# Kernel tuning notes

Measured on AMD Instinct MI355X. Metric: run time of the kernel, lower is better.

## Reference

```python
import jax, jax.numpy as jnp
import numpy as np

L, E, H, V = 12, 1024, 4096, 50277
LN_EPS = 9.999999747378752e-06  # tf float32 1e-5


def _layernorm(x, w, b):
    m = jnp.mean(x)
    xc = x - m
    return xc / jnp.sqrt(jnp.mean(xc * xc) + LN_EPS) * w + b


def setup_inputs() -> dict:
    key = jax.random.key(0)
    ks = jax.random.split(key, 32)
    f32 = jnp.float32

    def n(i, shape, s=0.02):
        return (jax.random.normal(ks[i], shape, f32) * s).astype(f32)

    inp = {
        "statea": n(0, (L, E), 0.3),
        "stateb": jax.random.uniform(ks[1], (L, E), f32),
        "statec": jax.random.uniform(ks[2], (L, E), f32),
        "stated": n(3, (L, E), 0.3),
        "preprocess": n(4, (V, E), 0.5),
        "ln1w": 1.0 + n(5, (L, E), 0.05),
        "ln1b": n(6, (L, E), 0.05),
        "ln2w": 1.0 + n(7, (L, E), 0.05),
        "ln2b": n(8, (L, E), 0.05),
        "att_key": n(9, (L, E, E)),
        "att_receptance": n(10, (L, E, E)),
        "att_value": n(11, (L, E, E)),
        "kktk": jax.random.uniform(ks[12], (L, E), f32),
        "vvtv": jax.random.uniform(ks[13], (L, E), f32),
        "rrtr": jax.random.uniform(ks[14], (L, E), f32),
        "time_first": n(15, (L, E), 0.2),
        "time_decay": n(16, (L, E), 0.2) - 1.0,
        "outputvv": n(17, (L, E, E)),
        "time_mix_k_ffn": jax.random.uniform(ks[18], (L, E), f32),
        "time_mix_r_ffn": jax.random.uniform(ks[19], (L, E), f32),
        "key_ffn": n(20, (L, H, E)),
        "receptance_ffn": n(21, (L, E, E)),
        "value_ffn": n(22, (L, E, H)),
        "post0": 1.0 + n(23, (E,), 0.05),
        "post1": n(24, (E,), 0.05),
        "post2": n(25, (V, E)),
        "token": 123,
    }
    return inp


def _forward(statea, stateb, statec, stated, preprocess, ln1w, ln1b, ln2w, ln2b,
             att_key, att_receptance, att_value, kktk, vvtv, rrtr, time_first,
             time_decay, outputvv, time_mix_k_ffn, time_mix_r_ffn, key_ffn,
             receptance_ffn, value_ffn, post0, post1, post2, token):
    x0 = preprocess[token]  # [E]

    def step(x, p):
        (sa, sb, sc, sd, l1w, l1b, l2w, l2b, ak, ar, av, kk, vv, rr,
         tfirst, tdecay, ovv, tmk_m, tmr_m, kf, rf, vf) = p
        xy = _layernorm(x, l1w, l1b)
        # WKV time-mixing (single step): mat-vecs + exp-decay state recursion
        k = jnp.exp(ak @ (xy + kk * sa))        # [E]
        v = av @ (xy + vv * sa)                 # [E]
        r = jnp.exp(ar @ (xy + rr * sa)) + 1.0  # [E]
        etf = jnp.exp(tfirst)
        w = sb + etf * k * v
        d = sc * r + etf * k * r
        mvv = ovv @ (w / (d + 0.001))           # [E]
        sxx = x + mvv
        aaa = xy
        etd = jnp.exp(tdecay)
        bbb = sb * etd + k * v
        ccc = sc * etd + k
        # channel-mixing FFN
        xx = _layernorm(sxx, l2w, l2b)
        kma = kf @ (xx + tmk_m * sd)            # [H]
        km = jnp.square(jnp.maximum(kma, 0.0))
        rt = jnp.exp(rf @ (xx + tmr_m * sd)) + 1.0  # [E]
        x_new = sxx + (vf @ km) / rt
        ddd = xx
        return x_new, (aaa, bbb, ccc, ddd)

    xs = (statea, stateb, statec, stated, ln1w, ln1b, ln2w, ln2b, att_key,
          att_receptance, att_value, kktk, vvtv, rrtr, time_first, time_decay,
          outputvv, time_mix_k_ffn, time_mix_r_ffn, key_ffn, receptance_ffn,
          value_ffn)
    xL, (aaa, bbb, ccc, ddd) = jax.lax.scan(step, x0, xs)
    logits = post2 @ _layernorm(xL, post0, post1)  # [V]
    return logits, aaa, bbb, ccc, ddd


def reference(statea, stateb, statec, stated, preprocess, ln1w, ln1b, ln2w, ln2b,
              att_key, att_receptance, att_value, kktk, vvtv, rrtr, time_first,
              time_decay, outputvv, time_mix_k_ffn, time_mix_r_ffn, key_ffn,
              receptance_ffn, value_ffn, post0, post1, post2, token):
    return _forward(statea, stateb, statec, stated, preprocess, ln1w, ln1b,
                    ln2w, ln2b, att_key, att_receptance, att_value, kktk, vvtv,
                    rrtr, time_first, time_decay, outputvv, time_mix_k_ffn,
                    time_mix_r_ffn, key_ffn, receptance_ffn, value_ffn, post0,
                    post1, post2, token)
```

## Files before the change

kernel.cpp:

```cpp
#include <hip/hip_runtime.h>
#include <math.h>


constexpr int E = 1024;
constexpr int H = 4096;
constexpr int V = 50277;
constexpr int L = 12;
constexpr int NBLK = 256;
constexpr int NTHR = 512;
constexpr float LN_EPS = 9.999999747378752e-06f;

#define SCOPE_AGENT __HIP_MEMORY_SCOPE_AGENT

__device__ __forceinline__ void cstoref(float *p, float v) {
  __hip_atomic_store(p, v, __ATOMIC_RELAXED, SCOPE_AGENT);
}
__device__ __forceinline__ void cstoreu(unsigned *p, unsigned v) {
  __hip_atomic_store(p, v, __ATOMIC_RELAXED, SCOPE_AGENT);
}
__device__ __forceinline__ unsigned cloadu(const unsigned *p) {
  return __hip_atomic_load(p, __ATOMIC_RELAXED, SCOPE_AGENT);
}
__device__ __forceinline__ float2 cload2(const float *p) {
  union { unsigned long long u; float2 f; } c;
  c.u = __hip_atomic_load((const unsigned long long *)p, __ATOMIC_RELAXED, SCOPE_AGENT);
  return c.f;
}

__device__ __forceinline__ void lds_sync() {
  __builtin_amdgcn_sched_barrier(0);
  asm volatile("s_waitcnt lgkmcnt(0)" ::: "memory");
  __builtin_amdgcn_s_barrier();
  __builtin_amdgcn_sched_barrier(0);
}

struct Args {
  const float *statea, *stateb, *statec, *stated, *pre;
  const float *ln1w, *ln1b, *ln2w, *ln2b;
  const float *ak, *ar, *av, *kk, *vv, *rr, *tf, *td, *ovv;
  const float *tmk, *tmr, *kf, *rf, *vf;
  const float *post0, *post1, *post2;
  const int *token;
  float *out;
  float *ws;
  unsigned *flags;
};

__device__ __forceinline__ void bar_arrive(const Args &a, unsigned ep, int blk) {
  __syncthreads();
  if (threadIdx.x == 0) cstoreu(&a.flags[blk * 32], ep);
  __builtin_amdgcn_sched_barrier(0);
}

__device__ __forceinline__ void bar_spin(const Args &a, unsigned ep) {
  __builtin_amdgcn_sched_barrier(0);
  if (threadIdx.x < NBLK) {
    while (cloadu(&a.flags[threadIdx.x * 32]) < ep)
      __builtin_amdgcn_s_sleep(2);
  }
  __builtin_amdgcn_s_barrier();
  __builtin_amdgcn_sched_barrier(0);
}

__device__ __forceinline__ float wred(float v) {
#pragma unroll
  for (int off = 32; off; off >>= 1) v += __shfl_down(v, off, 64);
  return v;
}

__device__ __forceinline__ float dot4(float4 w, float4 x) {
  return w.x * x.x + w.y * x.y + w.z * x.z + w.w * x.w;
}

__device__ __forceinline__ float2 block_stats_v(float2 v, float *s_x, float *s_red,
                                                int tid, int lane, int wid) {
  reinterpret_cast<float2 *>(s_x)[tid] = v;
  float s = v.x + v.y, s2 = v.x * v.x + v.y * v.y;
#pragma unroll
  for (int off = 32; off; off >>= 1) {
    s += __shfl_down(s, off, 64);
    s2 += __shfl_down(s2, off, 64);
  }
  if (lane == 0) { s_red[wid] = s; s_red[8 + wid] = s2; }
  lds_sync();
  float ts = 0.f, ts2 = 0.f;
#pragma unroll
  for (int i = 0; i < 8; ++i) { ts += s_red[i]; ts2 += s_red[8 + i]; }
  float m = ts * (1.0f / E);
  float var = ts2 * (1.0f / E) - m * m;
  return make_float2(m, rsqrtf(var + LN_EPS));
}

__device__ __forceinline__ void loadrow(float4 *d, const float4 *P, int r, int lane) {
  const float4 *p = P + (size_t)r * 256;
  d[0] = p[lane]; d[1] = p[lane + 64]; d[2] = p[lane + 128]; d[3] = p[lane + 192];
}

__global__ __launch_bounds__(NTHR) void rwkv_fused(Args a) {
  __shared__ __align__(16) float s_a[4096];
  __shared__ __align__(16) float s_x[1024];
  __shared__ __align__(16) float s_y[1024];
  __shared__ float s_pp[24];
  __shared__ float s_red[16];
  __shared__ float s_rt[4];

  const int tid = threadIdx.x;
  const int lane = tid & 63;
  const int wid = tid >> 6;
  const int blk = blockIdx.x;
  const int rloc = wid >> 1;
  const int h = wid & 1;
  const int grow = blk * 4 + rloc;
  const int b0h = h * 128 + lane;
  const int bv = h * 512 + lane;

  float *ws_u = a.ws, *ws_sxx = a.ws + 1024, *ws_x = a.ws + 2048, *ws_km = a.ws + 3072;
  float *out_logits = a.out;
  float *out_aaa = a.out + V;
  float *out_bbb = out_aaa + L * E;
  float *out_ccc = out_bbb + L * E;
  float *out_ddd = out_ccc + L * E;

  const int tok = a.token[0];
  const float *pre_row = a.pre + (size_t)tok * E;
  const float4 *s4a = reinterpret_cast<const float4 *>(s_a);

  unsigned ep = 1;

  float4 pw1[6];
  float2 e1w, e1b, e1sa, e1kk, e1vv, e1rr;
  float e_tf = 0.f, e_td = 0.f, e_sb = 0.f, e_sc = 0.f;

  {
    const float4 *kr = reinterpret_cast<const float4 *>(a.ak + (size_t)grow * E);
    const float4 *vr = reinterpret_cast<const float4 *>(a.av + (size_t)grow * E);
    const float4 *rr4 = reinterpret_cast<const float4 *>(a.ar + (size_t)grow * E);
    pw1[0] = kr[b0h]; pw1[1] = kr[b0h + 64];
    pw1[2] = vr[b0h]; pw1[3] = vr[b0h + 64];
    pw1[4] = rr4[b0h]; pw1[5] = rr4[b0h + 64];
    e1w = reinterpret_cast<const float2 *>(a.ln1w)[tid];
    e1b = reinterpret_cast<const float2 *>(a.ln1b)[tid];
    e1sa = reinterpret_cast<const float2 *>(a.statea)[tid];
    e1kk = reinterpret_cast<const float2 *>(a.kk)[tid];
    e1vv = reinterpret_cast<const float2 *>(a.vv)[tid];
    e1rr = reinterpret_cast<const float2 *>(a.rr)[tid];
    if (tid < 4) {
      size_t o = (size_t)blk * 4 + tid;
      e_tf = a.tf[o]; e_td = a.td[o]; e_sb = a.stateb[o]; e_sc = a.statec[o];
    }
  }

#pragma unroll 1
  for (int l = 0; l < L; ++l) {
    const size_t lE = (size_t)l * E;
    float4 pw2[2], pw3[10], pw4[8];
    float2 e3w, e3b, e3sd, e3tk, e3tr;

    {
      float2 v;
      if (l == 0) v = reinterpret_cast<const float2 *>(pre_row)[tid];
      else        v = cload2(ws_x + 2 * tid);
      {
        const float4 *orow = reinterpret_cast<const float4 *>(a.ovv + (lE + grow) * E);
        pw2[0] = orow[b0h]; pw2[1] = orow[b0h + 64];
        const float *kfb = a.kf + (size_t)l * H * E;
        const float4 *k0 = reinterpret_cast<const float4 *>(kfb + (size_t)(blk * 16 + wid) * E);
        pw3[0] = k0[lane];       pw3[1] = k0[lane + 64];
        pw3[2] = k0[lane + 128]; pw3[3] = k0[lane + 192];
      }
      float2 st = block_stats_v(v, s_x, s_red, tid, lane, wid);
      float2 xy = make_float2((v.x - st.x) * st.y * e1w.x + e1b.x,
                              (v.y - st.x) * st.y * e1w.y + e1b.y);
      reinterpret_cast<float2 *>(s_y)[tid] = xy;
      reinterpret_cast<float2 *>(s_a)[tid] =
          make_float2(xy.x + e1kk.x * e1sa.x, xy.y + e1kk.y * e1sa.y);
      reinterpret_cast<float2 *>(s_a + 1024)[tid] =
          make_float2(xy.x + e1vv.x * e1sa.x, xy.y + e1vv.y * e1sa.y);
      reinterpret_cast<float2 *>(s_a + 2048)[tid] =
          make_float2(xy.x + e1rr.x * e1sa.x, xy.y + e1rr.y * e1sa.y);
      lds_sync();
      float accK = dot4(pw1[0], s4a[b0h]) + dot4(pw1[1], s4a[b0h + 64]);
      float accV = dot4(pw1[2], s4a[256 + b0h]) + dot4(pw1[3], s4a[256 + b0h + 64]);
      float accR = dot4(pw1[4], s4a[512 + b0h]) + dot4(pw1[5], s4a[512 + b0h + 64]);
      accK = wred(accK); accV = wred(accV); accR = wred(accR);
      if (lane == 0) {
        s_pp[wid * 3 + 0] = accK;
        s_pp[wid * 3 + 1] = accV;
        s_pp[wid * 3 + 2] = accR;
      }
      lds_sync();
      if (tid < 4) {
        size_t o = lE + blk * 4 + tid;
        float K = s_pp[(2 * tid) * 3] + s_pp[(2 * tid + 1) * 3];
        float Vv = s_pp[(2 * tid) * 3 + 1] + s_pp[(2 * tid + 1) * 3 + 1];
        float R = s_pp[(2 * tid) * 3 + 2] + s_pp[(2 * tid + 1) * 3 + 2];
        float kx = expf(K), rx = expf(R) + 1.0f;
        float etf = expf(e_tf), etd = expf(e_td);
        float w_ = e_sb + etf * kx * Vv;
        float d_ = e_sc * rx + etf * kx * rx;
        cstoref(&ws_u[blk * 4 + tid], w_ / (d_ + 0.001f));
        out_bbb[o] = e_sb * etd + kx * Vv;
        out_ccc[o] = e_sc * etd + kx;
        out_aaa[o] = s_y[blk * 4 + tid];
      }
    }
    bar_arrive(a, ep, blk);
    {
      const float *kfb = a.kf + (size_t)l * H * E;
      const float4 *k1 = reinterpret_cast<const float4 *>(kfb + (size_t)(blk * 16 + 8 + wid) * E);
      pw3[4] = k1[lane];       pw3[5] = k1[lane + 64];
      pw3[6] = k1[lane + 128]; pw3[7] = k1[lane + 192];
    }
    bar_spin(a, ep); ++ep;

    {
      float2 u2 = cload2(ws_u + 2 * tid);
      {
        const float4 *rrow = reinterpret_cast<const float4 *>(a.rf + (lE + grow) * E);
        pw3[8] = rrow[b0h]; pw3[9] = rrow[b0h + 64];
        e3w = reinterpret_cast<const float2 *>(a.ln2w + lE)[tid];
        e3b = reinterpret_cast<const float2 *>(a.ln2b + lE)[tid];
        e3sd = reinterpret_cast<const float2 *>(a.stated + lE)[tid];
        e3tk = reinterpret_cast<const float2 *>(a.tmk + lE)[tid];
        e3tr = reinterpret_cast<const float2 *>(a.tmr + lE)[tid];
        const float4 *vrow = reinterpret_cast<const float4 *>(a.vf + (lE + grow) * H);
        pw4[0] = vrow[bv];       pw4[1] = vrow[bv + 64];
        pw4[2] = vrow[bv + 128]; pw4[3] = vrow[bv + 192];
      }
      reinterpret_cast<float2 *>(s_a)[tid] = u2;
      lds_sync();
      float acc = dot4(pw2[0], s4a[b0h]) + dot4(pw2[1], s4a[b0h + 64]);
      acc = wred(acc);
      if (lane == 0) s_pp[wid] = acc;
      lds_sync();
      if (tid < 4) {
        float sxx = s_x[blk * 4 + tid] + s_pp[2 * tid] + s_pp[2 * tid + 1];
        cstoref(&ws_sxx[blk * 4 + tid], sxx);
      }
    }
    bar_arrive(a, ep, blk);
    {
      const float4 *vrow = reinterpret_cast<const float4 *>(a.vf + (lE + grow) * H);
      pw4[4] = vrow[bv + 256]; pw4[5] = vrow[bv + 320];
      pw4[6] = vrow[bv + 384]; pw4[7] = vrow[bv + 448];
    }
    bar_spin(a, ep); ++ep;

    {
      float2 vsx = cload2(ws_sxx + 2 * tid);
      if (l + 1 < L) {
        const size_t nE = (size_t)(l + 1) * E;
        const float4 *kr = reinterpret_cast<const float4 *>(a.ak + (nE + grow) * E);
        const float4 *vr = reinterpret_cast<const float4 *>(a.av + (nE + grow) * E);
        const float4 *rr4 = reinterpret_cast<const float4 *>(a.ar + (nE + grow) * E);
        pw1[0] = kr[b0h]; pw1[1] = kr[b0h + 64];
        pw1[2] = vr[b0h]; pw1[3] = vr[b0h + 64];
        pw1[4] = rr4[b0h]; pw1[5] = rr4[b0h + 64];
        e1w = reinterpret_cast<const float2 *>(a.ln1w + nE)[tid];
        e1b = reinterpret_cast<const float2 *>(a.ln1b + nE)[tid];
        e1sa = reinterpret_cast<const float2 *>(a.statea + nE)[tid];
        e1kk = reinterpret_cast<const float2 *>(a.kk + nE)[tid];
        e1vv = reinterpret_cast<const float2 *>(a.vv + nE)[tid];
        e1rr = reinterpret_cast<const float2 *>(a.rr + nE)[tid];
        if (tid < 4) {
          size_t o = nE + blk * 4 + tid;
          e_tf = a.tf[o]; e_td = a.td[o]; e_sb = a.stateb[o]; e_sc = a.statec[o];
        }
      } else {
        e1w = reinterpret_cast<const float2 *>(a.post0)[tid];
        e1b = reinterpret_cast<const float2 *>(a.post1)[tid];
      }
      float2 st = block_stats_v(vsx, s_x, s_red, tid, lane, wid);
      float2 xx = make_float2((vsx.x - st.x) * st.y * e3w.x + e3b.x,
                              (vsx.y - st.x) * st.y * e3w.y + e3b.y);
      reinterpret_cast<float2 *>(s_y)[tid] = xx;
      reinterpret_cast<float2 *>(s_a)[tid] =
          make_float2(xx.x + e3tk.x * e3sd.x, xx.y + e3tk.y * e3sd.y);
      reinterpret_cast<float2 *>(s_a + 1024)[tid] =
          make_float2(xx.x + e3tr.x * e3sd.x, xx.y + e3tr.y * e3sd.y);
      lds_sync();
      float k0 = dot4(pw3[0], s4a[lane]) + dot4(pw3[1], s4a[lane + 64]) +
                 dot4(pw3[2], s4a[lane + 128]) + dot4(pw3[3], s4a[lane + 192]);
      float k1 = dot4(pw3[4], s4a[lane]) + dot4(pw3[5], s4a[lane + 64]) +
                 dot4(pw3[6], s4a[lane + 128]) + dot4(pw3[7], s4a[lane + 192]);
      float ar_ = dot4(pw3[8], s4a[256 + b0h]) + dot4(pw3[9], s4a[256 + b0h + 64]);
      k0 = wred(k0); k1 = wred(k1); ar_ = wred(ar_);
      if (lane == 0) {
        float t0 = fmaxf(k0, 0.f), t1v = fmaxf(k1, 0.f);
        cstoref(&ws_km[blk * 16 + wid], t0 * t0);
        cstoref(&ws_km[blk * 16 + 8 + wid], t1v * t1v);
        s_pp[wid] = ar_;
      }
      lds_sync();
      if (tid < 4) {
        s_rt[tid] = expf(s_pp[2 * tid] + s_pp[2 * tid + 1]) + 1.0f;
        out_ddd[lE + blk * 4 + tid] = s_y[blk * 4 + tid];
      }
    }
    bar_arrive(a, ep, blk);
    bar_spin(a, ep); ++ep;

    {
      float2 k0a = cload2(ws_km + 4 * tid);
      float2 k0b = cload2(ws_km + 4 * tid + 2);
      float2 k1a = cload2(ws_km + 2048 + 4 * tid);
      float2 k1b = cload2(ws_km + 2048 + 4 * tid + 2);
      reinterpret_cast<float2 *>(s_a)[2 * tid] = k0a;
      reinterpret_cast<float2 *>(s_a)[2 * tid + 1] = k0b;
      reinterpret_cast<float2 *>(s_a)[1024 + 2 * tid] = k1a;
      reinterpret_cast<float2 *>(s_a)[1024 + 2 * tid + 1] = k1b;
      lds_sync();
      float acc = dot4(pw4[0], s4a[bv]) + dot4(pw4[1], s4a[bv + 64]) +
                  dot4(pw4[2], s4a[bv + 128]) + dot4(pw4[3], s4a[bv + 192]) +
                  dot4(pw4[4], s4a[bv + 256]) + dot4(pw4[5], s4a[bv + 320]) +
                  dot4(pw4[6], s4a[bv + 384]) + dot4(pw4[7], s4a[bv + 448]);
      acc = wred(acc);
      if (lane == 0) s_pp[wid] = acc;
      lds_sync();
      if (tid < 4) {
        float xn = s_x[blk * 4 + tid] + (s_pp[2 * tid] + s_pp[2 * tid + 1]) / s_rt[tid];
        cstoref(&ws_x[blk * 4 + tid], xn);
      }
    }
    bar_arrive(a, ep, blk);
    bar_spin(a, ep); ++ep;
  }

  {
    float2 v = cload2(ws_x + 2 * tid);
    float2 st = block_stats_v(v, s_x, s_red, tid, lane, wid);
    reinterpret_cast<float2 *>(s_a)[tid] =
        make_float2((v.x - st.x) * st.y * e1w.x + e1b.x,
                    (v.y - st.x) * st.y * e1w.y + e1b.y);
    lds_sync();

    const float4 *P2 = reinterpret_cast<const float4 *>(a.post2);
    const int gw = blk * 8 + wid;
    int r0 = gw, r1 = gw + 2048;
    float4 A0[4], A1[4];
    loadrow(A0, P2, r0, lane);
    loadrow(A1, P2, r1 < V ? r1 : r0, lane);
    while (true) {
      int n0 = r0 + 4096, n1 = n0 + 2048;
      bool more = n0 < V;
      float4 B0[4], B1[4];
      if (more) {
        loadrow(B0, P2, n0, lane);
        loadrow(B1, P2, n1 < V ? n1 : n0, lane);
      }
      float a0 = dot4(A0[0], s4a[lane]) + dot4(A0[1], s4a[lane + 64]) +
                 dot4(A0[2], s4a[lane + 128]) + dot4(A0[3], s4a[lane + 192]);
      float a1 = dot4(A1[0], s4a[lane]) + dot4(A1[1], s4a[lane + 64]) +
                 dot4(A1[2], s4a[lane + 128]) + dot4(A1[3], s4a[lane + 192]);
      a0 = wred(a0); a1 = wred(a1);
      if (lane == 0) {
        out_logits[r0] = a0;
        if (r1 < V) out_logits[r1] = a1;
      }
      if (!more) break;
#pragma unroll
      for (int q = 0; q < 4; ++q) { A0[q] = B0[q]; A1[q] = B1[q]; }
      r0 = n0; r1 = n1;
    }
  }
}

extern "C" void kernel_launch(void *const *d_in, const int *in_sizes, int n_in,
                              void *d_out, int out_size, void *d_ws, size_t ws_size,
                              hipStream_t stream) {
  (void)in_sizes; (void)n_in; (void)out_size; (void)ws_size;
  Args a;
  a.statea = (const float *)d_in[0];
  a.stateb = (const float *)d_in[1];
  a.statec = (const float *)d_in[2];
  a.stated = (const float *)d_in[3];
  a.pre    = (const float *)d_in[4];
  a.ln1w   = (const float *)d_in[5];
  a.ln1b   = (const float *)d_in[6];
  a.ln2w   = (const float *)d_in[7];
  a.ln2b   = (const float *)d_in[8];
  a.ak     = (const float *)d_in[9];
  a.ar     = (const float *)d_in[10];
  a.av     = (const float *)d_in[11];
  a.kk     = (const float *)d_in[12];
  a.vv     = (const float *)d_in[13];
  a.rr     = (const float *)d_in[14];
  a.tf     = (const float *)d_in[15];
  a.td     = (const float *)d_in[16];
  a.ovv    = (const float *)d_in[17];
  a.tmk    = (const float *)d_in[18];
  a.tmr    = (const float *)d_in[19];
  a.kf     = (const float *)d_in[20];
  a.rf     = (const float *)d_in[21];
  a.vf     = (const float *)d_in[22];
  a.post0  = (const float *)d_in[23];
  a.post1  = (const float *)d_in[24];
  a.post2  = (const float *)d_in[25];
  a.token  = (const int *)d_in[26];
  a.out    = (float *)d_out;

  a.flags  = (unsigned *)d_ws;
  a.ws     = (float *)((char *)d_ws + 32768);

  hipMemsetAsync(d_ws, 0, 32768, stream);
  rwkv_fused<<<NBLK, NTHR, 0, stream>>>(a);
}
```

Before: 266.8 us.

## Replace grid flag barriers with epoch-tagged data words and partial LN stats

Drops the per-phase grid barrier (flag arrive plus spin over all blocks). Each published value now carries a 64-bit word with its epoch in the high half, so consumers poll only the exact data they need until it is current. Blocks also publish partial sums and sums of squares for the residual vectors, so layernorm statistics come from the gathered partials without a second block reduction. Weight prefetch placement changes, and launch bounds now request two blocks per CU. This removes barrier round trips but doubles the size of every exchanged word and adds polling traffic on many addresses.

```diff
diff --git a/kernel.cpp b/kernel.cpp
--- a/kernel.cpp
+++ b/kernel.cpp
@@ -1,6 +1,8 @@
 #include <hip/hip_runtime.h>
 #include <math.h>
 
+
+typedef unsigned long long u64;
 
 constexpr int E = 1024;
 constexpr int H = 4096;
@@ -12,26 +14,23 @@
 
 #define SCOPE_AGENT __HIP_MEMORY_SCOPE_AGENT
 
-__device__ __forceinline__ void cstoref(float *p, float v) {
+__device__ __forceinline__ u64 aload(const u64 *p) {
+  return __hip_atomic_load(p, __ATOMIC_RELAXED, SCOPE_AGENT);
+}
+__device__ __forceinline__ void astore(u64 *p, u64 v) {
   __hip_atomic_store(p, v, __ATOMIC_RELAXED, SCOPE_AGENT);
 }
-__device__ __forceinline__ void cstoreu(unsigned *p, unsigned v) {
-  __hip_atomic_store(p, v, __ATOMIC_RELAXED, SCOPE_AGENT);
-}
-__device__ __forceinline__ unsigned cloadu(const unsigned *p) {
-  return __hip_atomic_load(p, __ATOMIC_RELAXED, SCOPE_AGENT);
-}
-__device__ __forceinline__ float2 cload2(const float *p) {
-  union { unsigned long long u; float2 f; } c;
-  c.u = __hip_atomic_load((const unsigned long long *)p, __ATOMIC_RELAXED, SCOPE_AGENT);
-  return c.f;
+__device__ __forceinline__ u64 mkw(unsigned ep, float f) {
+  return ((u64)ep << 32) | (u64)__float_as_uint(f);
+}
+__device__ __forceinline__ float wpay(u64 v) { return __uint_as_float((unsigned)v); }
+__device__ __forceinline__ bool freshw(u64 v, unsigned ep) {
+  return (unsigned)(v >> 32) == ep;
 }
 
 __device__ __forceinline__ void lds_sync() {
-  __builtin_amdgcn_sched_barrier(0);
   asm volatile("s_waitcnt lgkmcnt(0)" ::: "memory");
   __builtin_amdgcn_s_barrier();
-  __builtin_amdgcn_sched_barrier(0);
 }
 
 struct Args {
@@ -42,25 +41,8 @@
   const float *post0, *post1, *post2;
   const int *token;
   float *out;
-  float *ws;
-  unsigned *flags;
+  u64 *wu, *wsx, *ssx, *wkm, *wx, *sxs;
 };
-
-__device__ __forceinline__ void bar_arrive(const Args &a, unsigned ep, int blk) {
-  __syncthreads();
-  if (threadIdx.x == 0) cstoreu(&a.flags[blk * 32], ep);
-  __builtin_amdgcn_sched_barrier(0);
-}
-
-__device__ __forceinline__ void bar_spin(const Args &a, unsigned ep) {
-  __builtin_amdgcn_sched_barrier(0);
-  if (threadIdx.x < NBLK) {
-    while (cloadu(&a.flags[threadIdx.x * 32]) < ep)
-      __builtin_amdgcn_s_sleep(2);
-  }
-  __builtin_amdgcn_s_barrier();
-  __builtin_amdgcn_sched_barrier(0);
-}
 
 __device__ __forceinline__ float wred(float v) {
 #pragma unroll
@@ -72,36 +54,115 @@
   return w.x * x.x + w.y * x.y + w.z * x.z + w.w * x.w;
 }
 
-__device__ __forceinline__ float2 block_stats_v(float2 v, float *s_x, float *s_red,
-                                                int tid, int lane, int wid) {
-  reinterpret_cast<float2 *>(s_x)[tid] = v;
-  float s = v.x + v.y, s2 = v.x * v.x + v.y * v.y;
-#pragma unroll
-  for (int off = 32; off; off >>= 1) {
-    s += __shfl_down(s, off, 64);
-    s2 += __shfl_down(s2, off, 64);
-  }
-  if (lane == 0) { s_red[wid] = s; s_red[8 + wid] = s2; }
+__device__ __forceinline__ float2 gather2(const u64 *wd, unsigned ep, int tid) {
+  const u64 *p = wd + 2 * tid;
+  u64 a0 = aload(p), a1 = aload(p + 1);
+  while (!(freshw(a0, ep) & freshw(a1, ep))) {
+    __builtin_amdgcn_s_sleep(1);
+    a0 = aload(p); a1 = aload(p + 1);
+  }
+  return make_float2(wpay(a0), wpay(a1));
+}
+
+__device__ __forceinline__ void gather2s(const u64 *wd, const u64 *st, unsigned ep,
+                                         int tid, float2 &v, float &sp) {
+  const u64 *p = wd + 2 * tid;
+  const u64 *q = st + tid;
+  u64 a0 = aload(p), a1 = aload(p + 1), a2 = aload(q);
+  while (!(freshw(a0, ep) & freshw(a1, ep) & freshw(a2, ep))) {
+    __builtin_amdgcn_s_sleep(1);
+    a0 = aload(p); a1 = aload(p + 1); a2 = aload(q);
+  }
+  v = make_float2(wpay(a0), wpay(a1));
+  sp = wpay(a2);
+}
+
+__device__ __forceinline__ void gather8(const u64 *wd, unsigned ep, int tid,
+                                        float4 &f0, float4 &f1) {
+  const u64 *p = wd + 8 * tid;
+  u64 b0, b1, b2, b3, b4, b5, b6, b7;
+  for (;;) {
+    b0 = aload(p);     b1 = aload(p + 1); b2 = aload(p + 2); b3 = aload(p + 3);
+    b4 = aload(p + 4); b5 = aload(p + 5); b6 = aload(p + 6); b7 = aload(p + 7);
+    bool ok = freshw(b0, ep) & freshw(b1, ep) & freshw(b2, ep) & freshw(b3, ep) &
+              freshw(b4, ep) & freshw(b5, ep) & freshw(b6, ep) & freshw(b7, ep);
+    if (ok) break;
+    __builtin_amdgcn_s_sleep(1);
+  }
+  f0 = make_float4(wpay(b0), wpay(b1), wpay(b2), wpay(b3));
+  f1 = make_float4(wpay(b4), wpay(b5), wpay(b6), wpay(b7));
+}
+
+__device__ __forceinline__ float2 stats_from_partials(float sp, float *s_red,
+                                                      int lane, int wid) {
+#pragma unroll
+  for (int m = 2; m <= 32; m <<= 1) sp += __shfl_xor(sp, m, 64);
+  if (lane < 2) s_red[wid * 2 + lane] = sp;
   lds_sync();
   float ts = 0.f, ts2 = 0.f;
 #pragma unroll
-  for (int i = 0; i < 8; ++i) { ts += s_red[i]; ts2 += s_red[8 + i]; }
+  for (int i = 0; i < 8; ++i) { ts += s_red[2 * i]; ts2 += s_red[2 * i + 1]; }
   float m = ts * (1.0f / E);
   float var = ts2 * (1.0f / E) - m * m;
   return make_float2(m, rsqrtf(var + LN_EPS));
 }
 
+__device__ __forceinline__ float2 stats_full(float2 v, float *s_red, int lane, int wid) {
+  float s = v.x + v.y, s2 = v.x * v.x + v.y * v.y;
+#pragma unroll
+  for (int m = 1; m <= 32; m <<= 1) {
+    s += __shfl_xor(s, m, 64);
+    s2 += __shfl_xor(s2, m, 64);
+  }
+  if (lane == 0) { s_red[wid * 2] = s; s_red[wid * 2 + 1] = s2; }
+  lds_sync();
+  float ts = 0.f, ts2 = 0.f;
+#pragma unroll
+  for (int i = 0; i < 8; ++i) { ts += s_red[2 * i]; ts2 += s_red[2 * i + 1]; }
+  float m = ts * (1.0f / E);
+  float var = ts2 * (1.0f / E) - m * m;
+  return make_float2(m, rsqrtf(var + LN_EPS));
+}
+
+struct P1B {
+  float4 w[6];
+  float2 lw, lb, sa, kk, vv, rr;
+  float tf, td, sb, sc;
+};
+
+__device__ __forceinline__ void load_p1(P1B &p, const Args &a, int l, int grow,
+                                        int b0h, int tid, int blk) {
+  const size_t lE = (size_t)l * E;
+  const float4 *kr = reinterpret_cast<const float4 *>(a.ak + (lE + grow) * E);
+  const float4 *vr = reinterpret_cast<const float4 *>(a.av + (lE + grow) * E);
+  const float4 *rr4 = reinterpret_cast<const float4 *>(a.ar + (lE + grow) * E);
+  p.w[0] = kr[b0h]; p.w[1] = kr[b0h + 64];
+  p.w[2] = vr[b0h]; p.w[3] = vr[b0h + 64];
+  p.w[4] = rr4[b0h]; p.w[5] = rr4[b0h + 64];
+  p.lw = reinterpret_cast<const float2 *>(a.ln1w + lE)[tid];
+  p.lb = reinterpret_cast<const float2 *>(a.ln1b + lE)[tid];
+  p.sa = reinterpret_cast<const float2 *>(a.statea + lE)[tid];
+  p.kk = reinterpret_cast<const float2 *>(a.kk + lE)[tid];
+  p.vv = reinterpret_cast<const float2 *>(a.vv + lE)[tid];
+  p.rr = reinterpret_cast<const float2 *>(a.rr + lE)[tid];
+  if (tid < 4) {
+    size_t o = lE + blk * 4 + tid;
+    p.tf = a.tf[o]; p.td = a.td[o]; p.sb = a.stateb[o]; p.sc = a.statec[o];
+  } else {
+    p.tf = 0.f; p.td = 0.f; p.sb = 0.f; p.sc = 1.f;
+  }
+}
+
 __device__ __forceinline__ void loadrow(float4 *d, const float4 *P, int r, int lane) {
   const float4 *p = P + (size_t)r * 256;
   d[0] = p[lane]; d[1] = p[lane + 64]; d[2] = p[lane + 128]; d[3] = p[lane + 192];
 }
 
-__global__ __launch_bounds__(NTHR) void rwkv_fused(Args a) {
+__global__ __launch_bounds__(NTHR, 2) void rwkv_fused(Args a) {
   __shared__ __align__(16) float s_a[4096];
   __shared__ __align__(16) float s_x[1024];
-  __shared__ __align__(16) float s_y[1024];
+  __shared__ float s_red[16];
   __shared__ float s_pp[24];
-  __shared__ float s_red[16];
   __shared__ float s_rt[4];
 
   const int tid = threadIdx.x;
@@ -114,7 +175,6 @@
   const int b0h = h * 128 + lane;
   const int bv = h * 512 + lane;
 
-  float *ws_u = a.ws, *ws_sxx = a.ws + 1024, *ws_x = a.ws + 2048, *ws_km = a.ws + 3072;
   float *out_logits = a.out;
   float *out_aaa = a.out + V;
   float *out_bbb = out_aaa + L * E;
@@ -125,63 +185,44 @@
   const float *pre_row = a.pre + (size_t)tok * E;
   const float4 *s4a = reinterpret_cast<const float4 *>(s_a);
 
-  unsigned ep = 1;
-
-  float4 pw1[6];
-  float2 e1w, e1b, e1sa, e1kk, e1vv, e1rr;
-  float e_tf = 0.f, e_td = 0.f, e_sb = 0.f, e_sc = 0.f;
-
-  {
-    const float4 *kr = reinterpret_cast<const float4 *>(a.ak + (size_t)grow * E);
-    const float4 *vr = reinterpret_cast<const float4 *>(a.av + (size_t)grow * E);
-    const float4 *rr4 = reinterpret_cast<const float4 *>(a.ar + (size_t)grow * E);
-    pw1[0] = kr[b0h]; pw1[1] = kr[b0h + 64];
-    pw1[2] = vr[b0h]; pw1[3] = vr[b0h + 64];
-    pw1[4] = rr4[b0h]; pw1[5] = rr4[b0h + 64];
-    e1w = reinterpret_cast<const float2 *>(a.ln1w)[tid];
-    e1b = reinterpret_cast<const float2 *>(a.ln1b)[tid];
-    e1sa = reinterpret_cast<const float2 *>(a.statea)[tid];
-    e1kk = reinterpret_cast<const float2 *>(a.kk)[tid];
-    e1vv = reinterpret_cast<const float2 *>(a.vv)[tid];
-    e1rr = reinterpret_cast<const float2 *>(a.rr)[tid];
-    if (tid < 4) {
-      size_t o = (size_t)blk * 4 + tid;
-      e_tf = a.tf[o]; e_td = a.td[o]; e_sb = a.stateb[o]; e_sc = a.statec[o];
-    }
-  }
+  P1B p1;
+  load_p1(p1, a, 0, grow, b0h, tid, blk);
 
 #pragma unroll 1
   for (int l = 0; l < L; ++l) {
     const size_t lE = (size_t)l * E;
-    float4 pw2[2], pw3[10], pw4[8];
+    const unsigned e1 = 4 * l + 1, e2 = 4 * l + 2, e3 = 4 * l + 3, e4 = 4 * l + 4;
+    float4 pwo[2], pw3[10], pw4[8];
     float2 e3w, e3b, e3sd, e3tk, e3tr;
 
     {
-      float2 v;
-      if (l == 0) v = reinterpret_cast<const float2 *>(pre_row)[tid];
-      else        v = cload2(ws_x + 2 * tid);
-      {
-        const float4 *orow = reinterpret_cast<const float4 *>(a.ovv + (lE + grow) * E);
-        pw2[0] = orow[b0h]; pw2[1] = orow[b0h + 64];
-        const float *kfb = a.kf + (size_t)l * H * E;
-        const float4 *k0 = reinterpret_cast<const float4 *>(kfb + (size_t)(blk * 16 + wid) * E);
-        pw3[0] = k0[lane];       pw3[1] = k0[lane + 64];
-        pw3[2] = k0[lane + 128]; pw3[3] = k0[lane + 192];
-      }
-      float2 st = block_stats_v(v, s_x, s_red, tid, lane, wid);
-      float2 xy = make_float2((v.x - st.x) * st.y * e1w.x + e1b.x,
-                              (v.y - st.x) * st.y * e1w.y + e1b.y);
-      reinterpret_cast<float2 *>(s_y)[tid] = xy;
+      float2 xv; float2 st;
+      if (l == 0) {
+        xv = reinterpret_cast<const float2 *>(pre_row)[tid];
+        reinterpret_cast<float2 *>(s_x)[tid] = xv;
+        st = stats_full(xv, s_red, lane, wid);
+      } else {
+        float sp;
+        gather2s(a.wx, a.sxs, 4 * l, tid, xv, sp);
+        reinterpret_cast<float2 *>(s_x)[tid] = xv;
+        st = stats_from_partials(sp, s_red, lane, wid);
+      }
+      float2 xy = make_float2((xv.x - st.x) * st.y * p1.lw.x + p1.lb.x,
+                              (xv.y - st.x) * st.y * p1.lw.y + p1.lb.y);
+      if ((tid >> 1) == blk) {
+        out_aaa[lE + 2 * tid] = xy.x;
+        out_aaa[lE + 2 * tid + 1] = xy.y;
+      }
       reinterpret_cast<float2 *>(s_a)[tid] =
-          make_float2(xy.x + e1kk.x * e1sa.x, xy.y + e1kk.y * e1sa.y);
+          make_float2(xy.x + p1.kk.x * p1.sa.x, xy.y + p1.kk.y * p1.sa.y);
       reinterpret_cast<float2 *>(s_a + 1024)[tid] =
-          make_float2(xy.x + e1vv.x * e1sa.x, xy.y + e1vv.y * e1sa.y);
+          make_float2(xy.x + p1.vv.x * p1.sa.x, xy.y + p1.vv.y * p1.sa.y);
       reinterpret_cast<float2 *>(s_a + 2048)[tid] =
-          make_float2(xy.x + e1rr.x * e1sa.x, xy.y + e1rr.y * e1sa.y);
-      lds_sync();
-      float accK = dot4(pw1[0], s4a[b0h]) + dot4(pw1[1], s4a[b0h + 64]);
-      float accV = dot4(pw1[2], s4a[256 + b0h]) + dot4(pw1[3], s4a[256 + b0h + 64]);
-      float accR = dot4(pw1[4], s4a[512 + b0h]) + dot4(pw1[5], s4a[512 + b0h + 64]);
+          make_float2(xy.x + p1.rr.x * p1.sa.x, xy.y + p1.rr.y * p1.sa.y);
+      lds_sync();
+      float accK = dot4(p1.w[0], s4a[b0h]) + dot4(p1.w[1], s4a[b0h + 64]);
+      float accV = dot4(p1.w[2], s4a[256 + b0h]) + dot4(p1.w[3], s4a[256 + b0h + 64]);
+      float accR = dot4(p1.w[4], s4a[512 + b0h]) + dot4(p1.w[5], s4a[512 + b0h + 64]);
       accK = wred(accK); accV = wred(accV); accR = wred(accR);
       if (lane == 0) {
         s_pp[wid * 3 + 0] = accK;
@@ -189,33 +230,46 @@
         s_pp[wid * 3 + 2] = accR;
       }
       lds_sync();
-      if (tid < 4) {
-        size_t o = lE + blk * 4 + tid;
-        float K = s_pp[(2 * tid) * 3] + s_pp[(2 * tid + 1) * 3];
-        float Vv = s_pp[(2 * tid) * 3 + 1] + s_pp[(2 * tid + 1) * 3 + 1];
-        float R = s_pp[(2 * tid) * 3 + 2] + s_pp[(2 * tid + 1) * 3 + 2];
+      {
+        const float4 *orow = reinterpret_cast<const float4 *>(a.ovv + (lE + grow) * E);
+        pwo[0] = orow[b0h]; pwo[1] = orow[b0h + 64];
+      }
+      if (wid == 0) {
+        int i = lane & 3;
+        float K = s_pp[(2 * i) * 3] + s_pp[(2 * i + 1) * 3];
+        float Vv = s_pp[(2 * i) * 3 + 1] + s_pp[(2 * i + 1) * 3 + 1];
+        float R = s_pp[(2 * i) * 3 + 2] + s_pp[(2 * i + 1) * 3 + 2];
         float kx = expf(K), rx = expf(R) + 1.0f;
-        float etf = expf(e_tf), etd = expf(e_td);
-        float w_ = e_sb + etf * kx * Vv;
-        float d_ = e_sc * rx + etf * kx * rx;
-        cstoref(&ws_u[blk * 4 + tid], w_ / (d_ + 0.001f));
-        out_bbb[o] = e_sb * etd + kx * Vv;
-        out_ccc[o] = e_sc * etd + kx;
-        out_aaa[o] = s_y[blk * 4 + tid];
+        float etf = expf(p1.tf), etd = expf(p1.td);
+        float w_ = p1.sb + etf * kx * Vv;
+        float d_ = p1.sc * rx + etf * kx * rx;
+        float uv = w_ / (d_ + 0.001f);
+        if (lane < 4) {
+          size_t o = lE + blk * 4 + lane;
+          astore(a.wu + blk * 4 + lane, mkw(e1, uv));
+          out_bbb[o] = p1.sb * etd + kx * Vv;
+          out_ccc[o] = p1.sc * etd + kx;
+        }
       }
     }
-    bar_arrive(a, ep, blk);
+
     {
-      const float *kfb = a.kf + (size_t)l * H * E;
-      const float4 *k1 = reinterpret_cast<const float4 *>(kfb + (size_t)(blk * 16 + 8 + wid) * E);
-      pw3[4] = k1[lane];       pw3[5] = k1[lane + 64];
-      pw3[6] = k1[lane + 128]; pw3[7] = k1[lane + 192];
-    }
-    bar_spin(a, ep); ++ep;
-
-    {
-      float2 u2 = cload2(ws_u + 2 * tid);
+      float2 u2 = gather2(a.wu, e1, tid);
+      reinterpret_cast<float2 *>(s_a)[tid] = u2;
+      lds_sync();
+      float acc = dot4(pwo[0], s4a[b0h]) + dot4(pwo[1], s4a[b0h + 64]);
+      float x4 = s_x[blk * 4 + (lane & 3)];
+      acc = wred(acc);
+      if (lane == 0) s_pp[wid] = acc;
+      lds_sync();
       {
+        const float *kfb = a.kf + (size_t)l * H * E;
+        const float4 *k0 = reinterpret_cast<const float4 *>(kfb + (size_t)(blk * 16 + wid) * E);
+        const float4 *k1 = reinterpret_cast<const float4 *>(kfb + (size_t)(blk * 16 + 8 + wid) * E);
+        pw3[0] = k0[lane];       pw3[1] = k0[lane + 64];
+        pw3[2] = k0[lane + 128]; pw3[3] = k0[lane + 192];
+        pw3[4] = k1[lane];       pw3[5] = k1[lane + 64];
+        pw3[6] = k1[lane + 128]; pw3[7] = k1[lane + 192];
         const float4 *rrow = reinterpret_cast<const float4 *>(a.rf + (lE + grow) * E);
         pw3[8] = rrow[b0h]; pw3[9] = rrow[b0h + 64];
         e3w = reinterpret_cast<const float2 *>(a.ln2w + lE)[tid];
@@ -223,115 +277,102 @@
         e3sd = reinterpret_cast<const float2 *>(a.stated + lE)[tid];
         e3tk = reinterpret_cast<const float2 *>(a.tmk + lE)[tid];
         e3tr = reinterpret_cast<const float2 *>(a.tmr + lE)[tid];
-        const float4 *vrow = reinterpret_cast<const float4 *>(a.vf + (lE + grow) * H);
-        pw4[0] = vrow[bv];       pw4[1] = vrow[bv + 64];
-        pw4[2] = vrow[bv + 128]; pw4[3] = vrow[bv + 192];
-      }
-      reinterpret_cast<float2 *>(s_a)[tid] = u2;
-      lds_sync();
-      float acc = dot4(pw2[0], s4a[b0h]) + dot4(pw2[1], s4a[b0h + 64]);
-      acc = wred(acc);
-      if (lane == 0) s_pp[wid] = acc;
-      lds_sync();
-      if (tid < 4) {
-        float sxx = s_x[blk * 4 + tid] + s_pp[2 * tid] + s_pp[2 * tid + 1];
-        cstoref(&ws_sxx[blk * 4 + tid], sxx);
+      }
+      if (wid == 0) {
+        int i = lane & 3;
+        float sxxv = x4 + s_pp[2 * i] + s_pp[2 * i + 1];
+        float s0 = __shfl(sxxv, 0), s1 = __shfl(sxxv, 1);
+        float s2v = __shfl(sxxv, 2), s3 = __shfl(sxxv, 3);
+        float sum = s0 + s1 + s2v + s3;
+        float ssq = s0 * s0 + s1 * s1 + s2v * s2v + s3 * s3;
+        if (lane < 4) astore(a.wsx + blk * 4 + lane, mkw(e2, sxxv));
+        if (lane == 0) astore(a.ssx + blk * 2 + 0, mkw(e2, sum));
+        if (lane == 1) astore(a.ssx + blk * 2 + 1, mkw(e2, ssq));
       }
     }
-    bar_arrive(a, ep, blk);
+
     {
-      const float4 *vrow = reinterpret_cast<const float4 *>(a.vf + (lE + grow) * H);
-      pw4[4] = vrow[bv + 256]; pw4[5] = vrow[bv + 320];
-      pw4[6] = vrow[bv + 384]; pw4[7] = vrow[bv + 448];
-    }
-    bar_spin(a, ep); ++ep;
-
-    {
-      float2 vsx = cload2(ws_sxx + 2 * tid);
-      if (l + 1 < L) {
-        const size_t nE = (size_t)(l + 1) * E;
-        const float4 *kr = reinterpret_cast<const float4 *>(a.ak + (nE + grow) * E);
-        const float4 *vr = reinterpret_cast<const float4 *>(a.av + (nE + grow) * E);
-        const float4 *rr4 = reinterpret_cast<const float4 *>(a.ar + (nE + grow) * E);
-        pw1[0] = kr[b0h]; pw1[1] = kr[b0h + 64];
-        pw1[2] = vr[b0h]; pw1[3] = vr[b0h + 64];
-        pw1[4] = rr4[b0h]; pw1[5] = rr4[b0h + 64];
-        e1w = reinterpret_cast<const float2 *>(a.ln1w + nE)[tid];
-        e1b = reinterpret_cast<const float2 *>(a.ln1b + nE)[tid];
-        e1sa = reinterpret_cast<const float2 *>(a.statea + nE)[tid];
-        e1kk = reinterpret_cast<const float2 *>(a.kk + nE)[tid];
-        e1vv = reinterpret_cast<const float2 *>(a.vv + nE)[tid];
-        e1rr = reinterpret_cast<const float2 *>(a.rr + nE)[tid];
-        if (tid < 4) {
-          size_t o = nE + blk * 4 + tid;
-          e_tf = a.tf[o]; e_td = a.td[o]; e_sb = a.stateb[o]; e_sc = a.statec[o];
-        }
-      } else {
-        e1w = reinterpret_cast<const float2 *>(a.post0)[tid];
-        e1b = reinterpret_cast<const float2 *>(a.post1)[tid];
-      }
-      float2 st = block_stats_v(vsx, s_x, s_red, tid, lane, wid);
-      float2 xx = make_float2((vsx.x - st.x) * st.y * e3w.x + e3b.x,
-                              (vsx.y - st.x) * st.y * e3w.y + e3b.y);
-      reinterpret_cast<float2 *>(s_y)[tid] = xx;
+      float2 sxv; float sp;
+      gather2s(a.wsx, a.ssx, e2, tid, sxv, sp);
+      reinterpret_cast<float2 *>(s_x)[tid] = sxv;
+      float2 st = stats_from_partials(sp, s_red, lane, wid);
+      float2 xx = make_float2((sxv.x - st.x) * st.y * e3w.x + e3b.x,
+                              (sxv.y - st.x) * st.y * e3w.y + e3b.y);
+      if ((tid >> 1) == blk) {
+        out_ddd[lE + 2 * tid] = xx.x;
+        out_ddd[lE + 2 * tid + 1] = xx.y;
+      }
       reinterpret_cast<float2 *>(s_a)[tid] =
           make_float2(xx.x + e3tk.x * e3sd.x, xx.y + e3tk.y * e3sd.y);
       reinterpret_cast<float2 *>(s_a + 1024)[tid] =
           make_float2(xx.x + e3tr.x * e3sd.x, xx.y + e3tr.y * e3sd.y);
       lds_sync();
-      float k0 = dot4(pw3[0], s4a[lane]) + dot4(pw3[1], s4a[lane + 64]) +
-                 dot4(pw3[2], s4a[lane + 128]) + dot4(pw3[3], s4a[lane + 192]);
-      float k1 = dot4(pw3[4], s4a[lane]) + dot4(pw3[5], s4a[lane + 64]) +
-                 dot4(pw3[6], s4a[lane + 128]) + dot4(pw3[7], s4a[lane + 192]);
+      float k0 = 0.f, k1 = 0.f;
+#pragma unroll
+      for (int it = 0; it < 4; ++it) {
+        float4 xv4 = s4a[it * 64 + lane];
+        k0 += dot4(pw3[it], xv4);
+        k1 += dot4(pw3[4 + it], xv4);
+      }
       float ar_ = dot4(pw3[8], s4a[256 + b0h]) + dot4(pw3[9], s4a[256 + b0h + 64]);
       k0 = wred(k0); k1 = wred(k1); ar_ = wred(ar_);
       if (lane == 0) {
-        float t0 = fmaxf(k0, 0.f), t1v = fmaxf(k1, 0.f);
-        cstoref(&ws_km[blk * 16 + wid], t0 * t0);
-        cstoref(&ws_km[blk * 16 + 8 + wid], t1v * t1v);
+        float t0 = fmaxf(k0, 0.f), t1 = fmaxf(k1, 0.f);
+        astore(a.wkm + blk * 16 + wid, mkw(e3, t0 * t0));
+        astore(a.wkm + blk * 16 + 8 + wid, mkw(e3, t1 * t1));
         s_pp[wid] = ar_;
       }
       lds_sync();
-      if (tid < 4) {
-        s_rt[tid] = expf(s_pp[2 * tid] + s_pp[2 * tid + 1]) + 1.0f;
-        out_ddd[lE + blk * 4 + tid] = s_y[blk * 4 + tid];
-      }
+      {
+        const float4 *vrow = reinterpret_cast<const float4 *>(a.vf + (lE + grow) * H);
+        pw4[0] = vrow[bv];       pw4[1] = vrow[bv + 64];
+        pw4[2] = vrow[bv + 128]; pw4[3] = vrow[bv + 192];
+        pw4[4] = vrow[bv + 256]; pw4[5] = vrow[bv + 320];
+        pw4[6] = vrow[bv + 384]; pw4[7] = vrow[bv + 448];
+      }
+      if (tid < 4) s_rt[tid] = expf(s_pp[2 * tid] + s_pp[2 * tid + 1]) + 1.0f;
     }
-    bar_arrive(a, ep, blk);
-    bar_spin(a, ep); ++ep;
 
     {
-      float2 k0a = cload2(ws_km + 4 * tid);
-      float2 k0b = cload2(ws_km + 4 * tid + 2);
-      float2 k1a = cload2(ws_km + 2048 + 4 * tid);
-      float2 k1b = cload2(ws_km + 2048 + 4 * tid + 2);
-      reinterpret_cast<float2 *>(s_a)[2 * tid] = k0a;
-      reinterpret_cast<float2 *>(s_a)[2 * tid + 1] = k0b;
-      reinterpret_cast<float2 *>(s_a)[1024 + 2 * tid] = k1a;
-      reinterpret_cast<float2 *>(s_a)[1024 + 2 * tid + 1] = k1b;
-      lds_sync();
-      float acc = dot4(pw4[0], s4a[bv]) + dot4(pw4[1], s4a[bv + 64]) +
-                  dot4(pw4[2], s4a[bv + 128]) + dot4(pw4[3], s4a[bv + 192]) +
-                  dot4(pw4[4], s4a[bv + 256]) + dot4(pw4[5], s4a[bv + 320]) +
-                  dot4(pw4[6], s4a[bv + 384]) + dot4(pw4[7], s4a[bv + 448]);
+      float4 f0, f1;
+      gather8(a.wkm, e3, tid, f0, f1);
+      reinterpret_cast<float4 *>(s_a)[2 * tid] = f0;
+      reinterpret_cast<float4 *>(s_a)[2 * tid + 1] = f1;
+      lds_sync();
+      float acc = 0.f;
+#pragma unroll
+      for (int it = 0; it < 8; ++it) acc += dot4(pw4[it], s4a[bv + it * 64]);
+      float sx4 = s_x[blk * 4 + (lane & 3)];
       acc = wred(acc);
       if (lane == 0) s_pp[wid] = acc;
       lds_sync();
-      if (tid < 4) {
-        float xn = s_x[blk * 4 + tid] + (s_pp[2 * tid] + s_pp[2 * tid + 1]) / s_rt[tid];
-        cstoref(&ws_x[blk * 4 + tid], xn);
+      if (l + 1 < L) {
+        load_p1(p1, a, l + 1, grow, b0h, tid, blk);
+      } else {
+        p1.lw = reinterpret_cast<const float2 *>(a.post0)[tid];
+        p1.lb = reinterpret_cast<const float2 *>(a.post1)[tid];
+      }
+      if (wid == 0) {
+        int i = lane & 3;
+        float xn = sx4 + (s_pp[2 * i] + s_pp[2 * i + 1]) / s_rt[i];
+        float s0 = __shfl(xn, 0), s1 = __shfl(xn, 1);
+        float s2v = __shfl(xn, 2), s3 = __shfl(xn, 3);
+        float sum = s0 + s1 + s2v + s3;
+        float ssq = s0 * s0 + s1 * s1 + s2v * s2v + s3 * s3;
+        if (lane < 4) astore(a.wx + blk * 4 + lane, mkw(e4, xn));
+        if (lane == 0) astore(a.sxs + blk * 2 + 0, mkw(e4, sum));
+        if (lane == 1) astore(a.sxs + blk * 2 + 1, mkw(e4, ssq));
       }
     }
-    bar_arrive(a, ep, blk);
-    bar_spin(a, ep); ++ep;
   }
 
   {
-    float2 v = cload2(ws_x + 2 * tid);
-    float2 st = block_stats_v(v, s_x, s_red, tid, lane, wid);
+    float2 xv; float sp;
+    gather2s(a.wx, a.sxs, 4 * L, tid, xv, sp);
+    float2 st = stats_from_partials(sp, s_red, lane, wid);
     reinterpret_cast<float2 *>(s_a)[tid] =
-        make_float2((v.x - st.x) * st.y * e1w.x + e1b.x,
-                    (v.y - st.x) * st.y * e1w.y + e1b.y);
+        make_float2((xv.x - st.x) * st.y * p1.lw.x + p1.lb.x,
+                    (xv.y - st.x) * st.y * p1.lw.y + p1.lb.y);
     lds_sync();
 
     const float4 *P2 = reinterpret_cast<const float4 *>(a.post2);
@@ -399,9 +440,13 @@
   a.token  = (const int *)d_in[26];
   a.out    = (float *)d_out;
 
-  a.flags  = (unsigned *)d_ws;
-  a.ws     = (float *)((char *)d_ws + 32768);
-
-  hipMemsetAsync(d_ws, 0, 32768, stream);
+  u64 *wb = (u64 *)d_ws;
+  a.wu  = wb;
+  a.wsx = wb + 1024;
+  a.ssx = wb + 2048;
+  a.wkm = wb + 2560;
+  a.wx  = wb + 6656;
+  a.sxs = wb + 7680;
+  hipMemsetAsync(d_ws, 0, 8192 * sizeof(u64), stream);
   rwkv_fused<<<NBLK, NTHR, 0, stream>>>(a);
 }
```

Measured after the change: 302.3 us. +13.3%, slower.
